# Optimization experiments

Hardware: AMD Instinct MI355X
Metric: run time of the kernel (lower is better)

The kernel has to match this reference:

```python
import jax, jax.numpy as jnp
import numpy as np

N_NODES = 50000
N_EDGES = 800000
NUM_GRAPHS = 128
KS = 5           # kernel_size per pseudo dim
K = KS * KS      # 25 spline weight matrices per layer


def spline_coeff(pseudo):
    """Open linear (degree-1) B-spline basis for 2-D pseudo coords in [0,1].
    Returns dense per-edge coefficients over the K=25 kernel slots: [E, K]."""
    pos = pseudo * (KS - 1)                      # [E,2]
    lo = jnp.clip(jnp.floor(pos).astype(jnp.int32), 0, KS - 2)
    frac = pos - lo.astype(pseudo.dtype)         # [E,2]
    i0, i1 = lo, lo + 1
    w0, w1 = 1.0 - frac, frac
    # 2^dim = 4 corner combinations, flat index = d0 + KS*d1
    idx = jnp.stack([i0[:, 0] + KS * i0[:, 1],
                     i0[:, 0] + KS * i1[:, 1],
                     i1[:, 0] + KS * i0[:, 1],
                     i1[:, 0] + KS * i1[:, 1]], axis=1)            # [E,4]
    w = jnp.stack([w0[:, 0] * w0[:, 1], w0[:, 0] * w1[:, 1],
                   w1[:, 0] * w0[:, 1], w1[:, 0] * w1[:, 1]], axis=1)  # [E,4]
    E = pseudo.shape[0]
    coeff = jnp.zeros((E, K), pseudo.dtype).at[jnp.arange(E)[:, None], idx].add(w)
    return coeff


def spline_conv(x, coeff, src, dst, W, root, bias):
    """SplineConv: gather src feats, spline-weighted transform, scatter-mean to dst,
    plus root weight and bias. x:[N,in], coeff:[E,K], W:[K,in,out]."""
    n = x.shape[0]
    x_src = x[src]                                # [E,in] gather
    m = coeff[:, 0:1] * (x_src @ W[0])            # [E,out]
    for k in range(1, K):                         # fixed small loop over K kernels
        m = m + coeff[:, k:k + 1] * (x_src @ W[k])
    agg = jax.ops.segment_sum(m, dst, num_segments=n)
    cnt = jax.ops.segment_sum(jnp.ones((src.shape[0],), x.dtype), dst, num_segments=n)
    agg = agg / jnp.maximum(cnt, 1.0)[:, None]    # mean aggregation (PyG default)
    return agg + x @ root + bias


def setup_inputs() -> dict:
    key = jax.random.key(0)
    ks = jax.random.split(key, 16)
    s = 0.1  # small init scale for numerical stability
    return {
        "x": jax.random.normal(ks[0], (N_NODES, 1), jnp.float32),
        "position": jax.random.uniform(ks[1], (N_NODES, 2), jnp.float32),
        "pseudo": jax.random.uniform(ks[2], (N_EDGES, 2), jnp.float32),
        "edge_index": jax.random.randint(ks[3], (2, N_EDGES), 0, N_NODES, jnp.int32),
        "batch": jnp.sort(jax.random.randint(ks[4], (N_NODES,), 0, NUM_GRAPHS, jnp.int32)),
        "W1": s * jax.random.normal(ks[5], (K, 1, 32), jnp.float32),
        "root1": s * jax.random.normal(ks[6], (1, 32), jnp.float32),
        "b1": jnp.zeros((32,), jnp.float32),
        "W2": s * jax.random.normal(ks[7], (K, 32, 64), jnp.float32),
        "root2": s * jax.random.normal(ks[8], (32, 64), jnp.float32),
        "b2": jnp.zeros((64,), jnp.float32),
        "W3": s * jax.random.normal(ks[9], (K, 64, 64), jnp.float32),
        "root3": s * jax.random.normal(ks[10], (64, 64), jnp.float32),
        "b3": jnp.zeros((64,), jnp.float32),
        "fc_w": s * jax.random.normal(ks[11], (64, 10), jnp.float32),
        "fc_b": jnp.zeros((10,), jnp.float32),
    }


def reference(x, position, pseudo, edge_index, batch,
              W1, root1, b1, W2, root2, b2, W3, root3, b3, fc_w, fc_b):
    # `position` is accepted but unused, matching the original forward.
    src, dst = edge_index[0], edge_index[1]
    coeff = spline_coeff(pseudo)
    h = jax.nn.elu(spline_conv(x, coeff, src, dst, W1, root1, b1))
    h = jax.nn.elu(spline_conv(h, coeff, src, dst, W2, root2, b2))
    h = jax.nn.elu(spline_conv(h, coeff, src, dst, W3, root3, b3))
    # scatter_mean pooling over batch indices -> [NUM_GRAPHS, 64]
    pooled = jax.ops.segment_sum(h, batch, num_segments=NUM_GRAPHS)
    gcnt = jax.ops.segment_sum(jnp.ones((h.shape[0],), h.dtype), batch,
                               num_segments=NUM_GRAPHS)
    pooled = pooled / jnp.maximum(gcnt, 1.0)[:, None]
    # dropout is identity in eval mode
    logits = pooled @ fc_w + fc_b
    return jax.nn.log_softmax(logits, axis=1)
```

## Files before the change

kernel.cpp:

```cpp
#include <hip/hip_runtime.h>

#define NN 50000
#define NE 800000
#define NG 128
#define NB_SCAN 196
#define PADW 0xC1000000u

typedef unsigned int uint;
typedef unsigned short ushort;
typedef __attribute__((ext_vector_type(8))) short short8;
typedef __attribute__((ext_vector_type(4))) float f32x4;
typedef __attribute__((ext_vector_type(16))) float f32x16;

__device__ __forceinline__ float bf2f(ushort u){ union{uint i; float f;} v; v.i=(uint)u<<16; return v.f; }
__device__ __forceinline__ ushort f2bf(float f){ union{float f; uint i;} v; v.f=f; return (ushort)((v.i + 0x7FFFu + ((v.i>>16)&1u))>>16); }
__device__ __forceinline__ int iswz(int i){ return i ^ ((i>>4)&3); }

__global__ void zero_k(int* hist, float* pooled, int* gcnt){
    int i = blockIdx.x*blockDim.x + threadIdx.x;
    if (i < NN) hist[i] = 0;
    if (i < NG*64) pooled[i] = 0.f;
    if (i < NG) gcnt[i] = 0;
}

__global__ void hist_k(const int* __restrict__ ei, int* __restrict__ hist){
    int e = blockIdx.x*blockDim.x + threadIdx.x;
    if (e < NE) atomicAdd(&hist[ei[NE + e]], 1);
}

__global__ __launch_bounds__(256) void scan1(const int* __restrict__ hist, int* __restrict__ bsum){
    __shared__ int sm[256];
    int t = threadIdx.x, i = blockIdx.x*256 + t;
    sm[t] = (i < NN) ? hist[i] : 0;
    __syncthreads();
    for (int o = 128; o > 0; o >>= 1){ if (t < o) sm[t] += sm[t+o]; __syncthreads(); }
    if (t == 0) bsum[blockIdx.x] = sm[0];
}
__global__ __launch_bounds__(256) void scan2(const int* __restrict__ bsum, int* __restrict__ bpre){
    __shared__ int sm[256];
    int t = threadIdx.x;
    int v = (t < NB_SCAN) ? bsum[t] : 0;
    sm[t] = v; __syncthreads();
    int acc = v;
    for (int o = 1; o < 256; o <<= 1){
        int u = (t >= o) ? sm[t-o] : 0; __syncthreads();
        acc += u; sm[t] = acc; __syncthreads();
    }
    if (t < NB_SCAN) bpre[t] = acc - v;
}
__global__ __launch_bounds__(256) void scan3(const int* __restrict__ hist, const int* __restrict__ bpre,
                                             int* __restrict__ offs, int* __restrict__ cursor,
                                             float* __restrict__ invc){
    __shared__ int sm[256];
    int t = threadIdx.x, b = blockIdx.x, i = b*256 + t;
    int v = (i < NN) ? hist[i] : 0;
    sm[t] = v; __syncthreads();
    int acc = v;
    for (int o = 1; o < 256; o <<= 1){
        int u = (t >= o) ? sm[t-o] : 0; __syncthreads();
        acc += u; sm[t] = acc; __syncthreads();
    }
    int excl = acc - v + bpre[b];
    if (i < NN){ offs[i] = excl; cursor[i] = excl; invc[i] = 1.0f/(float)max(v,1); }
    if (i == NN-1) offs[NN] = NE;
}

__global__ void scatter_k(const int* __restrict__ ei, const float* __restrict__ pseudo,
                          int* __restrict__ cursor, uint4* __restrict__ payA){
    int e = blockIdx.x*blockDim.x + threadIdx.x;
    if (e >= NE) return;
    float2 ps = *(const float2*)(pseudo + 2*(size_t)e);
    float px = ps.x * 4.0f, py = ps.y * 4.0f;
    int lx = min(max((int)floorf(px), 0), 3);
    int ly = min(max((int)floorf(py), 0), 3);
    uint meta = (uint)ei[e] | ((uint)lx<<16) | ((uint)ly<<18);
    int pos = atomicAdd(&cursor[ei[NE + e]], 1);
    payA[pos] = make_uint4(meta, __float_as_uint(px), __float_as_uint(py), 0u);
}

template<int IN>
__global__ void wprep_k(const float* __restrict__ W, const float* __restrict__ root, ushort* __restrict__ Bp){
    const int total = 26*IN*64;
    int tid = blockIdx.x*blockDim.x + threadIdx.x;
    if (tid >= total) return;
    int j    = tid & 7;
    int lane = (tid >> 3) & 63;
    int ctkt = tid >> 9;
    int ct   = ctkt & 3;
    int kt   = ctkt >> 2;
    int kk   = kt*32 + (lane>>4)*8 + j;
    int col  = ct*16 + (lane & 15);
    float v;
    if (kk < 25*IN){ int k = kk / IN; int i = kk % IN; v = W[((size_t)k*IN + i)*64 + col]; }
    else           { v = root[(size_t)(kk - 25*IN)*64 + col]; }
    Bp[tid] = f2bf(v);
}

__global__ __launch_bounds__(256) void reduce1_k(const float* __restrict__ x, const uint4* __restrict__ payA,
                                                 const int* __restrict__ offs, const float* __restrict__ invc,
                                                 const float* __restrict__ W1, const float* __restrict__ root1,
                                                 const float* __restrict__ b1, ushort* __restrict__ h1bf){
    __shared__ float w1s[25*32];
    for (int i = threadIdx.x; i < 25*32; i += 256) w1s[i] = W1[i];
    __syncthreads();
    int wid  = threadIdx.x >> 6;
    int lane = threadIdx.x & 63;
    int o    = lane & 31;
    int half = lane >> 5;
    int d    = blockIdx.x*4 + wid;
    int s = offs[d], e = offs[d+1];
    float acc = 0.f;
#define E1(QA, XS) { uint meta = (QA).x; \
    int lx = (meta>>16)&3, ly = (meta>>18)&3; \
    float px = __uint_as_float((QA).y), py = __uint_as_float((QA).z); \
    float fx = px - (float)lx, fy = py - (float)ly; \
    float gx = 1.f - fx, gy = 1.f - fy; \
    float wa = half ? fx*gy : gx*gy; \
    float wb = half ? fx*fy : gx*fy; \
    int ka = ly*5 + lx + half; \
    acc += (wa*w1s[ka*32 + o] + wb*w1s[(ka+5)*32 + o]) * (XS); }
    int p = s;
    for (; p + 4 <= e; p += 4){
        uint4 a0 = payA[p], a1 = payA[p+1], a2 = payA[p+2], a3 = payA[p+3];
        float x0 = x[a0.x & 0xFFFF], x1 = x[a1.x & 0xFFFF];
        float x2 = x[a2.x & 0xFFFF], x3 = x[a3.x & 0xFFFF];
        E1(a0, x0) E1(a1, x1) E1(a2, x2) E1(a3, x3)
    }
    for (; p < e; ++p){
        uint4 a0 = payA[p];
        float x0 = x[a0.x & 0xFFFF];
        E1(a0, x0)
    }
#undef E1
    acc += __shfl_xor(acc, 32);
    if (half == 0){
        float val = acc*invc[d] + x[d]*root1[o] + b1[o];
        val = val > 0.f ? val : expm1f(val);
        h1bf[(size_t)d*32 + o] = f2bf(val);
    }
}

#define WCALC(Q0, AH) { \
    float px_ = __uint_as_float((Q0).y), py_ = __uint_as_float((Q0).z); \
    float wx_ = fmaxf(1.f - fabsf(px_ - fi0), 0.f); \
    float wy_ = fmaxf(1.f - fabsf(py_ - fj0), 0.f); \
    (AH) = (short)f2bf(wx_ * wy_); }

#define STAGE(BUF, STEP) { \
    int rem_ = h - (STEP)*16; if (rem_ > 16) rem_ = 16; \
    if (lane < 16 && lane >= rem_) eA[w][BUF][lane] = PAD4; \
    if (lane < rem_){ \
        __builtin_amdgcn_global_load_lds( \
            (const __attribute__((address_space(1))) void*)(payA + (size_t)s + (STEP)*16 + lane), \
            (__attribute__((address_space(3))) void*)&eA[w][BUF][lane], 16, 0, 0); \
    } }

template<int MODE>
__global__ __launch_bounds__(512) void fused32(
        const ushort* __restrict__ hin, const uint4* __restrict__ payA,
        const int* __restrict__ offs, const float* __restrict__ invc,
        const ushort* __restrict__ Bp, const float* __restrict__ bias,
        const int* __restrict__ batch, ushort* __restrict__ hout,
        float* __restrict__ pooled, int* __restrict__ gcnt)
{
    constexpr int KT = 26, KH = 13;
    __shared__ __align__(16) ushort Sb[KT*512];
    __shared__ __align__(16) uint4 eA[8][2][16];
    __shared__ float red[1024];
    __shared__ float outS[1024];

    const int tid = threadIdx.x, lane = tid & 63, w = tid >> 6;
    const int ln31 = lane & 31, kg2 = lane >> 5;
    const int d0 = blockIdx.x * 16;
    const float fi0 = (float)(ln31 % 5), fj0 = (float)(ln31 / 5);
    const uint4 PAD4 = make_uint4(0u, PADW, PADW, 0u);

    for (int nn = 0; nn < 2; ++nn){
        const int node = w*2 + nn;
        const int d = d0 + node;
        int s = offs[d];
        int h = offs[d+1] - s;
        int steps = (h + 15) >> 4;

        f32x16 accH;
        #pragma unroll
        for (int q = 0; q < 16; ++q) accH[q] = 0.f;

        if (steps > 0) STAGE(0, 0)
        for (int ks = 0; ks < steps; ++ks){
            int cb = ks & 1;
            if (ks+1 < steps){
                STAGE(cb^1, ks+1)
                asm volatile("s_waitcnt vmcnt(1)" ::: "memory");
            } else {
                asm volatile("s_waitcnt vmcnt(0)" ::: "memory");
            }
            __builtin_amdgcn_sched_barrier(0);
            short8 ah; short8 bfv;
            #pragma unroll
            for (int j = 0; j < 8; ++j){
                uint4 q0 = eA[w][cb][kg2*8 + j];
                WCALC(q0, ah[j])
                bfv[j] = (short)hin[(size_t)(q0.x & 0xFFFFu)*32 + ln31];
            }
            accH = __builtin_amdgcn_mfma_f32_32x32x16_bf16(ah, bfv, accH, 0, 0, 0);
        }

        {
            float ic = invc[d];
            int jd  = ln31 & 7;
            int l3  = ln31 >> 3;
            #pragma unroll
            for (int reg = 0; reg < 16; ++reg){
                int r = (reg & 3) + 8*(reg >> 2) + 4*kg2;
                if (r < 25)
                    Sb[r*512 + iswz(l3*16 + node)*8 + jd] = f2bf(accH[reg]*ic);
            }
            if (lane < 32)
                Sb[25*512 + iswz(((lane>>3)&3)*16 + node)*8 + (lane&7)] = hin[(size_t)d*32 + lane];
        }
    }
    __syncthreads();

    {
        int ct = w & 3, kh = w >> 2;
        int c15 = lane & 15, kg = lane >> 4;
        int ig = iswz(lane);
        f32x4 a4 = {0.f,0.f,0.f,0.f};
        const ushort* bb = Bp + ct*512 + (size_t)lane*8;
        #pragma unroll
        for (int k = 0; k < KH; ++k){
            int kt = kh*KH + k;
            short8 a = *(const short8*)(Sb + kt*512 + ig*8);
            short8 b = *(const short8*)(bb + (size_t)kt*2048);
            a4 = __builtin_amdgcn_mfma_f32_16x16x32_bf16(a, b, a4, 0, 0, 0);
        }
        if (kh == 1){
            float* rr = red + (ct*64 + lane)*4;
            rr[0]=a4[0]; rr[1]=a4[1]; rr[2]=a4[2]; rr[3]=a4[3];
        }
        __syncthreads();
        if (kh == 0){
            const float* rr = red + (ct*64 + lane)*4;
            int col = ct*16 + c15;
            float bs = bias[col];
            #pragma unroll
            for (int jq = 0; jq < 4; ++jq){
                int r16 = kg*4 + jq;
                float v = a4[jq] + rr[jq] + bs;
                v = v > 0.f ? v : expm1f(v);
                if (MODE == 0) ((ushort*)outS)[r16*64 + col] = f2bf(v);
                else           outS[r16*64 + col] = v;
            }
        }
    }
    __syncthreads();

    if (MODE == 0){
        uint* dst = (uint*)(hout + (size_t)d0*64);
        dst[tid] = ((const uint*)outS)[tid];
    } else {
        if (w == 0){
            int c = lane;
            float run = 0.f; int gprev = batch[d0];
            for (int r = 0; r < 16; ++r){
                int g = batch[d0 + r];
                if (g != gprev){ atomicAdd(&pooled[gprev*64 + c], run); run = 0.f; gprev = g; }
                run += outS[r*64 + c];
            }
            atomicAdd(&pooled[gprev*64 + c], run);
        } else if (w == 1 && lane == 0){
            int cnt = 0; int gprev = batch[d0];
            for (int r = 0; r < 16; ++r){
                int g = batch[d0 + r];
                if (g != gprev){ atomicAdd(&gcnt[gprev], cnt); cnt = 0; gprev = g; }
                cnt++;
            }
            atomicAdd(&gcnt[gprev], cnt);
        }
    }
}

template<int MODE>
__global__ __launch_bounds__(512) void fused64(
        const ushort* __restrict__ hin, const uint4* __restrict__ payA,
        const int* __restrict__ offs, const float* __restrict__ invc,
        const ushort* __restrict__ Bp, const float* __restrict__ bias,
        const int* __restrict__ batch, ushort* __restrict__ hout,
        float* __restrict__ pooled, int* __restrict__ gcnt)
{
    constexpr int KT = 52, KH = 26;
    __shared__ __align__(16) ushort Sb[KT*512];
    __shared__ __align__(16) uint4 eA[8][2][16];
    __shared__ float red[1024];
    __shared__ float outS[1024];

    const int tid = threadIdx.x, lane = tid & 63, w = tid >> 6;
    const int ln31 = lane & 31, kg2 = lane >> 5;
    const int d0 = blockIdx.x * 16;
    const float fi0 = (float)(ln31 % 5), fj0 = (float)(ln31 / 5);
    const uint4 PAD4 = make_uint4(0u, PADW, PADW, 0u);

    for (int nn = 0; nn < 2; ++nn){
        const int node = w*2 + nn;
        const int d = d0 + node;
        int s = offs[d];
        int h = offs[d+1] - s;
        int steps = (h + 15) >> 4;

        f32x16 acc0, acc1;
        #pragma unroll
        for (int q = 0; q < 16; ++q){ acc0[q] = 0.f; acc1[q] = 0.f; }

        if (steps > 0) STAGE(0, 0)
        for (int ks = 0; ks < steps; ++ks){
            int cb = ks & 1;
            if (ks+1 < steps){
                STAGE(cb^1, ks+1)
                asm volatile("s_waitcnt vmcnt(1)" ::: "memory");
            } else {
                asm volatile("s_waitcnt vmcnt(0)" ::: "memory");
            }
            __builtin_amdgcn_sched_barrier(0);
            short8 ah; uint hx[8];
            #pragma unroll
            for (int j = 0; j < 8; ++j){
                uint4 q0 = eA[w][cb][kg2*8 + j];
                WCALC(q0, ah[j])
                hx[j] = *(const uint*)(hin + (size_t)(q0.x & 0xFFFFu)*64 + 2*ln31);
            }
            short8 b0, b1;
            #pragma unroll
            for (int j = 0; j < 8; ++j){
                b0[j] = (short)(ushort)hx[j];
                b1[j] = (short)(ushort)(hx[j] >> 16);
            }
            acc0 = __builtin_amdgcn_mfma_f32_32x32x16_bf16(ah, b0, acc0, 0, 0, 0);
            acc1 = __builtin_amdgcn_mfma_f32_32x32x16_bf16(ah, b1, acc1, 0, 0, 0);
        }

        {
            float ic = invc[d];
            int off0 = 2*ln31;
            int fhi  = ln31 >> 4;
            int kgp  = (off0 >> 3) & 3;
            int jd0  = off0 & 7;
            int gsl  = iswz(kgp*16 + node)*8;
            #pragma unroll
            for (int reg = 0; reg < 16; ++reg){
                int r = (reg & 3) + 8*(reg >> 2) + 4*kg2;
                if (r < 25){
                    int kt = r*2 + fhi;
                    uint pk = (uint)f2bf(acc0[reg]*ic) | ((uint)f2bf(acc1[reg]*ic) << 16);
                    *(uint*)(Sb + kt*512 + gsl + jd0) = pk;
                }
            }
            int f = lane;
            Sb[(50 + (f>>5))*512 + iswz(((f>>3)&3)*16 + node)*8 + (f&7)] = hin[(size_t)d*64 + f];
        }
    }
    __syncthreads();

    {
        int ct = w & 3, kh = w >> 2;
        int c15 = lane & 15, kg = lane >> 4;
        int ig = iswz(lane);
        f32x4 a4 = {0.f,0.f,0.f,0.f};
        const ushort* bb = Bp + ct*512 + (size_t)lane*8;
        #pragma unroll
        for (int k = 0; k < KH; ++k){
            int kt = kh*KH + k;
            short8 a = *(const short8*)(Sb + kt*512 + ig*8);
            short8 b = *(const short8*)(bb + (size_t)kt*2048);
            a4 = __builtin_amdgcn_mfma_f32_16x16x32_bf16(a, b, a4, 0, 0, 0);
        }
        if (kh == 1){
            float* rr = red + (ct*64 + lane)*4;
            rr[0]=a4[0]; rr[1]=a4[1]; rr[2]=a4[2]; rr[3]=a4[3];
        }
        __syncthreads();
        if (kh == 0){
            const float* rr = red + (ct*64 + lane)*4;
            int col = ct*16 + c15;
            float bs = bias[col];
            #pragma unroll
            for (int jq = 0; jq < 4; ++jq){
                int r16 = kg*4 + jq;
                float v = a4[jq] + rr[jq] + bs;
                v = v > 0.f ? v : expm1f(v);
                if (MODE == 0) ((ushort*)outS)[r16*64 + col] = f2bf(v);
                else           outS[r16*64 + col] = v;
            }
        }
    }
    __syncthreads();

    if (MODE == 0){
        uint* dst = (uint*)(hout + (size_t)d0*64);
        dst[tid] = ((const uint*)outS)[tid];
    } else {
        if (w == 0){
            int c = lane;
            float run = 0.f; int gprev = batch[d0];
            for (int r = 0; r < 16; ++r){
                int g = batch[d0 + r];
                if (g != gprev){ atomicAdd(&pooled[gprev*64 + c], run); run = 0.f; gprev = g; }
                run += outS[r*64 + c];
            }
            atomicAdd(&pooled[gprev*64 + c], run);
        } else if (w == 1 && lane == 0){
            int cnt = 0; int gprev = batch[d0];
            for (int r = 0; r < 16; ++r){
                int g = batch[d0 + r];
                if (g != gprev){ atomicAdd(&gcnt[gprev], cnt); cnt = 0; gprev = g; }
                cnt++;
            }
            atomicAdd(&gcnt[gprev], cnt);
        }
    }
}

__global__ __launch_bounds__(128) void head_k(const float* __restrict__ pooled, const int* __restrict__ gcnt,
                                              const float* __restrict__ fcw, const float* __restrict__ fcb,
                                              float* __restrict__ out){
    int g = threadIdx.x;
    if (g >= NG) return;
    float inv = 1.0f / fmaxf((float)gcnt[g], 1.0f);
    float logits[10];
    #pragma unroll
    for (int c = 0; c < 10; ++c) logits[c] = fcb[c];
    for (int o = 0; o < 64; ++o){
        float m = pooled[g*64 + o] * inv;
        #pragma unroll
        for (int c = 0; c < 10; ++c) logits[c] += m * fcw[o*10 + c];
    }
    float mx = logits[0];
    #pragma unroll
    for (int c = 1; c < 10; ++c) mx = fmaxf(mx, logits[c]);
    float ssum = 0.f;
    #pragma unroll
    for (int c = 0; c < 10; ++c) ssum += expf(logits[c] - mx);
    float lse = logf(ssum) + mx;
    #pragma unroll
    for (int c = 0; c < 10; ++c) out[g*10 + c] = logits[c] - lse;
}

extern "C" void kernel_launch(void* const* d_in, const int* in_sizes, int n_in,
                              void* d_out, int out_size, void* d_ws, size_t ws_size,
                              hipStream_t stream) {
    const float* x      = (const float*)d_in[0];
    const float* pseudo = (const float*)d_in[2];
    const int*   ei     = (const int*)  d_in[3];
    const int*   batch  = (const int*)  d_in[4];
    const float* W1     = (const float*)d_in[5];
    const float* root1  = (const float*)d_in[6];
    const float* b1     = (const float*)d_in[7];
    const float* W2     = (const float*)d_in[8];
    const float* root2  = (const float*)d_in[9];
    const float* b2     = (const float*)d_in[10];
    const float* W3     = (const float*)d_in[11];
    const float* root3  = (const float*)d_in[12];
    const float* b3     = (const float*)d_in[13];
    const float* fcw    = (const float*)d_in[14];
    const float* fcb    = (const float*)d_in[15];
    float* out = (float*)d_out;

    char* ws = (char*)d_ws;
    size_t off = 0;
    auto alloc = [&](size_t bytes)->char*{ char* p = ws + off; off += (bytes + 255) / 256 * 256; return p; };
    uint4*  payA   = (uint4*) alloc((size_t)NE*16);
    ushort* h1bf   = (ushort*)alloc((size_t)NN*32*2);
    ushort* h2bf   = (ushort*)alloc((size_t)NN*64*2);
    int*    hist   = (int*)   alloc((size_t)NN*4);
    int*    offs   = (int*)   alloc((size_t)(NN+1)*4);
    int*    cursor = (int*)   alloc((size_t)NN*4);
    float*  invc   = (float*) alloc((size_t)NN*4);
    int*    bsum   = (int*)   alloc((size_t)NB_SCAN*4);
    int*    bpre   = (int*)   alloc((size_t)NB_SCAN*4);
    ushort* Bp2    = (ushort*)alloc((size_t)26*2048*2);
    ushort* Bp3    = (ushort*)alloc((size_t)52*2048*2);
    float*  pooled = (float*) alloc((size_t)NG*64*4);
    int*    gcnt   = (int*)   alloc((size_t)NG*4);
    (void)ws_size; (void)in_sizes; (void)n_in; (void)out_size;

    zero_k   <<<NB_SCAN, 256, 0, stream>>>(hist, pooled, gcnt);
    hist_k   <<<(NE+255)/256, 256, 0, stream>>>(ei, hist);
    scan1    <<<NB_SCAN, 256, 0, stream>>>(hist, bsum);
    scan2    <<<1, 256, 0, stream>>>(bsum, bpre);
    scan3    <<<NB_SCAN, 256, 0, stream>>>(hist, bpre, offs, cursor, invc);
    scatter_k<<<(NE+255)/256, 256, 0, stream>>>(ei, pseudo, cursor, payA);
    wprep_k<32><<<(26*32*64 + 255)/256, 256, 0, stream>>>(W2, root2, Bp2);
    wprep_k<64><<<(26*64*64 + 255)/256, 256, 0, stream>>>(W3, root3, Bp3);
    reduce1_k<<<NN/4, 256, 0, stream>>>(x, payA, offs, invc, W1, root1, b1, h1bf);
    fused32<0><<<NN/16, 512, 0, stream>>>(h1bf, payA, offs, invc, Bp2, b2, batch, h2bf, pooled, gcnt);
    fused64<1><<<NN/16, 512, 0, stream>>>(h2bf, payA, offs, invc, Bp3, b3, batch, h2bf, pooled, gcnt);
    head_k   <<<1, 128, 0, stream>>>(pooled, gcnt, fcw, fcb, out);
}
```

Before: 280.2 us.

## Sort nodes into degree buckets to balance per-block work in fused layers

```diff
diff --git a/kernel.cpp b/kernel.cpp
--- a/kernel.cpp
+++ b/kernel.cpp
@@ -16,11 +16,12 @@
 __device__ __forceinline__ ushort f2bf(float f){ union{float f; uint i;} v; v.f=f; return (ushort)((v.i + 0x7FFFu + ((v.i>>16)&1u))>>16); }
 __device__ __forceinline__ int iswz(int i){ return i ^ ((i>>4)&3); }
 
-__global__ void zero_k(int* hist, float* pooled, int* gcnt){
+__global__ void zero_k(int* hist, float* pooled, int* gcnt, int* bcnt){
     int i = blockIdx.x*blockDim.x + threadIdx.x;
     if (i < NN) hist[i] = 0;
     if (i < NG*64) pooled[i] = 0.f;
     if (i < NG) gcnt[i] = 0;
+    if (i < 16) bcnt[i] = 0;
 }
 
 __global__ void hist_k(const int* __restrict__ ei, int* __restrict__ hist){
@@ -50,7 +51,7 @@
 }
 __global__ __launch_bounds__(256) void scan3(const int* __restrict__ hist, const int* __restrict__ bpre,
                                              int* __restrict__ offs, int* __restrict__ cursor,
-                                             float* __restrict__ invc){
+                                             float* __restrict__ invc, int* __restrict__ bcnt){
     __shared__ int sm[256];
     int t = threadIdx.x, b = blockIdx.x, i = b*256 + t;
     int v = (i < NN) ? hist[i] : 0;
@@ -61,8 +62,26 @@
         acc += u; sm[t] = acc; __syncthreads();
     }
     int excl = acc - v + bpre[b];
-    if (i < NN){ offs[i] = excl; cursor[i] = excl; invc[i] = 1.0f/(float)max(v,1); }
+    if (i < NN){
+        offs[i] = excl; cursor[i] = excl; invc[i] = 1.0f/(float)max(v,1);
+        int sv = (v + 15) >> 4; if (sv > 15) sv = 15;
+        atomicAdd(&bcnt[sv], 1);
+    }
     if (i == NN-1) offs[NN] = NE;
+}
+
+__global__ void bpfx(const int* __restrict__ bcnt, int* __restrict__ bcur){
+    if (threadIdx.x == 0){
+        int run = 0;
+        for (int k = 0; k < 16; ++k){ bcur[k] = run; run += bcnt[k]; }
+    }
+}
+__global__ void bscat(const int* __restrict__ hist, int* __restrict__ bcur, int* __restrict__ perm){
+    int d = blockIdx.x*blockDim.x + threadIdx.x;
+    if (d >= NN) return;
+    int sv = (hist[d] + 15) >> 4; if (sv > 15) sv = 15;
+    int pos = atomicAdd(&bcur[sv], 1);
+    perm[pos] = d;
 }
 
 __global__ void scatter_k(const int* __restrict__ ei, const float* __restrict__ pseudo,
@@ -159,6 +178,7 @@
 __global__ __launch_bounds__(512) void fused32(
         const ushort* __restrict__ hin, const uint4* __restrict__ payA,
         const int* __restrict__ offs, const float* __restrict__ invc,
+        const int* __restrict__ perm,
         const ushort* __restrict__ Bp, const float* __restrict__ bias,
         const int* __restrict__ batch, ushort* __restrict__ hout,
         float* __restrict__ pooled, int* __restrict__ gcnt)
@@ -168,6 +188,7 @@
     __shared__ __align__(16) uint4 eA[8][2][16];
     __shared__ float red[1024];
     __shared__ float outS[1024];
+    __shared__ int pdS[16];
 
     const int tid = threadIdx.x, lane = tid & 63, w = tid >> 6;
     const int ln31 = lane & 31, kg2 = lane >> 5;
@@ -175,9 +196,11 @@
     const float fi0 = (float)(ln31 % 5), fj0 = (float)(ln31 / 5);
     const uint4 PAD4 = make_uint4(0u, PADW, PADW, 0u);
 
+    if (tid < 16) pdS[tid] = perm[d0 + tid];
+
     for (int nn = 0; nn < 2; ++nn){
         const int node = w*2 + nn;
-        const int d = d0 + node;
+        const int d = perm[d0 + node];
         int s = offs[d];
         int h = offs[d+1] - s;
         int steps = (h + 15) >> 4;
@@ -257,26 +280,15 @@
     __syncthreads();
 
     if (MODE == 0){
-        uint* dst = (uint*)(hout + (size_t)d0*64);
-        dst[tid] = ((const uint*)outS)[tid];
+        int row = tid >> 5, c2 = tid & 31;
+        ((uint*)hout)[(size_t)pdS[row]*32 + c2] = ((const uint*)outS)[tid];
     } else {
         if (w == 0){
-            int c = lane;
-            float run = 0.f; int gprev = batch[d0];
-            for (int r = 0; r < 16; ++r){
-                int g = batch[d0 + r];
-                if (g != gprev){ atomicAdd(&pooled[gprev*64 + c], run); run = 0.f; gprev = g; }
-                run += outS[r*64 + c];
-            }
-            atomicAdd(&pooled[gprev*64 + c], run);
-        } else if (w == 1 && lane == 0){
-            int cnt = 0; int gprev = batch[d0];
-            for (int r = 0; r < 16; ++r){
-                int g = batch[d0 + r];
-                if (g != gprev){ atomicAdd(&gcnt[gprev], cnt); cnt = 0; gprev = g; }
-                cnt++;
-            }
-            atomicAdd(&gcnt[gprev], cnt);
+            #pragma unroll
+            for (int r = 0; r < 16; ++r)
+                atomicAdd(&pooled[batch[pdS[r]]*64 + lane], outS[r*64 + lane]);
+        } else if (w == 1 && lane < 16){
+            atomicAdd(&gcnt[batch[pdS[lane]]], 1);
         }
     }
 }
@@ -285,6 +297,7 @@
 __global__ __launch_bounds__(512) void fused64(
         const ushort* __restrict__ hin, const uint4* __restrict__ payA,
         const int* __restrict__ offs, const float* __restrict__ invc,
+        const int* __restrict__ perm,
         const ushort* __restrict__ Bp, const float* __restrict__ bias,
         const int* __restrict__ batch, ushort* __restrict__ hout,
         float* __restrict__ pooled, int* __restrict__ gcnt)
@@ -294,6 +307,7 @@
     __shared__ __align__(16) uint4 eA[8][2][16];
     __shared__ float red[1024];
     __shared__ float outS[1024];
+    __shared__ int pdS[16];
 
     const int tid = threadIdx.x, lane = tid & 63, w = tid >> 6;
     const int ln31 = lane & 31, kg2 = lane >> 5;
@@ -301,9 +315,11 @@
     const float fi0 = (float)(ln31 % 5), fj0 = (float)(ln31 / 5);
     const uint4 PAD4 = make_uint4(0u, PADW, PADW, 0u);
 
+    if (tid < 16) pdS[tid] = perm[d0 + tid];
+
     for (int nn = 0; nn < 2; ++nn){
         const int node = w*2 + nn;
-        const int d = d0 + node;
+        const int d = perm[d0 + node];
         int s = offs[d];
         int h = offs[d+1] - s;
         int steps = (h + 15) >> 4;
@@ -396,26 +412,15 @@
     __syncthreads();
 
     if (MODE == 0){
-        uint* dst = (uint*)(hout + (size_t)d0*64);
-        dst[tid] = ((const uint*)outS)[tid];
+        int row = tid >> 5, c2 = tid & 31;
+        ((uint*)hout)[(size_t)pdS[row]*32 + c2] = ((const uint*)outS)[tid];
     } else {
         if (w == 0){
-            int c = lane;
-            float run = 0.f; int gprev = batch[d0];
-            for (int r = 0; r < 16; ++r){
-                int g = batch[d0 + r];
-                if (g != gprev){ atomicAdd(&pooled[gprev*64 + c], run); run = 0.f; gprev = g; }
-                run += outS[r*64 + c];
-            }
-            atomicAdd(&pooled[gprev*64 + c], run);
-        } else if (w == 1 && lane == 0){
-            int cnt = 0; int gprev = batch[d0];
-            for (int r = 0; r < 16; ++r){
-                int g = batch[d0 + r];
-                if (g != gprev){ atomicAdd(&gcnt[gprev], cnt); cnt = 0; gprev = g; }
-                cnt++;
-            }
-            atomicAdd(&gcnt[gprev], cnt);
+            #pragma unroll
+            for (int r = 0; r < 16; ++r)
+                atomicAdd(&pooled[batch[pdS[r]]*64 + lane], outS[r*64 + lane]);
+        } else if (w == 1 && lane < 16){
+            atomicAdd(&gcnt[batch[pdS[lane]]], 1);
         }
     }
 }
@@ -477,22 +482,27 @@
     float*  invc   = (float*) alloc((size_t)NN*4);
     int*    bsum   = (int*)   alloc((size_t)NB_SCAN*4);
     int*    bpre   = (int*)   alloc((size_t)NB_SCAN*4);
+    int*    bcnt   = (int*)   alloc((size_t)16*4);
+    int*    bcur   = (int*)   alloc((size_t)16*4);
+    int*    perm   = (int*)   alloc((size_t)NN*4);
     ushort* Bp2    = (ushort*)alloc((size_t)26*2048*2);
     ushort* Bp3    = (ushort*)alloc((size_t)52*2048*2);
     float*  pooled = (float*) alloc((size_t)NG*64*4);
     int*    gcnt   = (int*)   alloc((size_t)NG*4);
     (void)ws_size; (void)in_sizes; (void)n_in; (void)out_size;
 
-    zero_k   <<<NB_SCAN, 256, 0, stream>>>(hist, pooled, gcnt);
+    zero_k   <<<NB_SCAN, 256, 0, stream>>>(hist, pooled, gcnt, bcnt);
     hist_k   <<<(NE+255)/256, 256, 0, stream>>>(ei, hist);
     scan1    <<<NB_SCAN, 256, 0, stream>>>(hist, bsum);
     scan2    <<<1, 256, 0, stream>>>(bsum, bpre);
-    scan3    <<<NB_SCAN, 256, 0, stream>>>(hist, bpre, offs, cursor, invc);
+    scan3    <<<NB_SCAN, 256, 0, stream>>>(hist, bpre, offs, cursor, invc, bcnt);
+    bpfx     <<<1, 64, 0, stream>>>(bcnt, bcur);
+    bscat    <<<NB_SCAN, 256, 0, stream>>>(hist, bcur, perm);
     scatter_k<<<(NE+255)/256, 256, 0, stream>>>(ei, pseudo, cursor, payA);
     wprep_k<32><<<(26*32*64 + 255)/256, 256, 0, stream>>>(W2, root2, Bp2);
     wprep_k<64><<<(26*64*64 + 255)/256, 256, 0, stream>>>(W3, root3, Bp3);
     reduce1_k<<<NN/4, 256, 0, stream>>>(x, payA, offs, invc, W1, root1, b1, h1bf);
-    fused32<0><<<NN/16, 512, 0, stream>>>(h1bf, payA, offs, invc, Bp2, b2, batch, h2bf, pooled, gcnt);
-    fused64<1><<<NN/16, 512, 0, stream>>>(h2bf, payA, offs, invc, Bp3, b3, batch, h2bf, pooled, gcnt);
+    fused32<0><<<NN/16, 512, 0, stream>>>(h1bf, payA, offs, invc, perm, Bp2, b2, batch, h2bf, pooled, gcnt);
+    fused64<1><<<NN/16, 512, 0, stream>>>(h2bf, payA, offs, invc, perm, Bp3, b3, batch, h2bf, pooled, gcnt);
     head_k   <<<1, 128, 0, stream>>>(pooled, gcnt, fcw, fcb, out);
 }
```

After: 1.094 ms. 3.9x slower.
